# Kernel tuning notes

Measured on AMD Instinct MI355X. Metric: run time of the kernel, lower is better.

## Reference

```python
import jax, jax.numpy as jnp
import numpy as np

TEMPERATURE = 0.07
EPS = 1e-12  # matches torch F.normalize default


def _l2_normalize(x):
    # torch F.normalize: x / max(||x||_2, eps)
    norm = jnp.sqrt(jnp.sum(x * x, axis=-1, keepdims=True))
    return x / jnp.maximum(norm, EPS)


def setup_inputs() -> dict:
    key = jax.random.key(0)
    k1, k2, k3 = jax.random.split(key, 3)
    B, N, D = 4096, 127, 256
    anchor = jax.random.normal(k1, (B, D), dtype=jnp.float32)
    positive = jax.random.normal(k2, (B, D), dtype=jnp.float32)
    negatives = jax.random.normal(k3, (B, N, D), dtype=jnp.float32)
    return {"anchor": anchor, "positive": positive, "negatives": negatives}


def reference(anchor, positive, negatives):
    a = _l2_normalize(anchor)          # [B, D]
    p = _l2_normalize(positive)        # [B, D]
    n = _l2_normalize(negatives)       # [B, N, D]
    pos_scores = jnp.sum(a * p, axis=-1, keepdims=True)   # [B, 1]
    neg_scores = jnp.einsum("bd,bnd->bn", a, n)           # [B, N]
    logits = jnp.concatenate([pos_scores, neg_scores], axis=1) / TEMPERATURE
    # cross-entropy with label 0 for every row
    loss = jnp.mean(jax.nn.logsumexp(logits, axis=-1) - logits[:, 0])
    return loss
```

## Files before the change

kernel.cpp:

```cpp
#include <hip/hip_runtime.h>
#include <math.h>


namespace {
constexpr int B = 4096;
constexpr int N = 127;
constexpr int D = 256;
constexpr float INV_TEMP = 1.0f / 0.07f;
constexpr float EPS = 1e-12f;

__device__ __forceinline__ float wave_reduce_sum(float v) {
    #pragma unroll
    for (int off = 32; off > 0; off >>= 1) v += __shfl_xor(v, off, 64);
    return v;
}

__device__ __forceinline__ float wave_reduce_max(float v) {
    #pragma unroll
    for (int off = 32; off > 0; off >>= 1) v = fmaxf(v, __shfl_xor(v, off, 64));
    return v;
}
}

__global__ __launch_bounds__(256) void infonce_rows(
    const float* __restrict__ anchor,
    const float* __restrict__ positive,
    const float* __restrict__ negatives,
    float* __restrict__ row_loss)
{
    const int b    = blockIdx.x;
    const int tid  = threadIdx.x;
    const int wave = tid >> 6;
    const int lane = tid & 63;

    __shared__ float scores[1 + N];

    const float4 a4 = *reinterpret_cast<const float4*>(
        anchor + (size_t)b * D + lane * 4);
    float asq = a4.x * a4.x + a4.y * a4.y + a4.z * a4.z + a4.w * a4.w;
    asq = wave_reduce_sum(asq);
    const float ainv = 1.0f / fmaxf(sqrtf(asq), EPS);
    const float4 ah = make_float4(a4.x * ainv, a4.y * ainv,
                                  a4.z * ainv, a4.w * ainv);

    if (wave == 0) {
        const float4 p4 = *reinterpret_cast<const float4*>(
            positive + (size_t)b * D + lane * 4);
        float psq  = p4.x * p4.x + p4.y * p4.y + p4.z * p4.z + p4.w * p4.w;
        float pdot = ah.x * p4.x + ah.y * p4.y + ah.z * p4.z + ah.w * p4.w;
        psq  = wave_reduce_sum(psq);
        pdot = wave_reduce_sum(pdot);
        if (lane == 0)
            scores[0] = pdot / fmaxf(sqrtf(psq), EPS);
    }

    const float* nrow_base = negatives + (size_t)b * N * D;
    for (int j = wave; j < N; j += 4) {
        const float4 n4 = *reinterpret_cast<const float4*>(
            nrow_base + (size_t)j * D + lane * 4);
        float nsq  = n4.x * n4.x + n4.y * n4.y + n4.z * n4.z + n4.w * n4.w;
        float ndot = ah.x * n4.x + ah.y * n4.y + ah.z * n4.z + ah.w * n4.w;
        nsq  = wave_reduce_sum(nsq);
        ndot = wave_reduce_sum(ndot);
        if (lane == 0)
            scores[1 + j] = ndot / fmaxf(sqrtf(nsq), EPS);
    }
    __syncthreads();

    if (wave == 0) {
        const float s0 = scores[lane]      * INV_TEMP;
        const float s1 = scores[lane + 64] * INV_TEMP;
        float m = wave_reduce_max(fmaxf(s0, s1));
        float e = expf(s0 - m) + expf(s1 - m);
        e = wave_reduce_sum(e);
        if (lane == 0)
            row_loss[b] = m + logf(e) - scores[0] * INV_TEMP;
    }
}

__global__ __launch_bounds__(256) void reduce_mean(
    const float* __restrict__ row_loss, float* __restrict__ out)
{
    __shared__ float wsum[4];
    const int tid  = threadIdx.x;
    const int wave = tid >> 6;
    const int lane = tid & 63;

    float s = 0.0f;
    for (int i = tid; i < B; i += 256) s += row_loss[i];
    s = wave_reduce_sum(s);
    if (lane == 0) wsum[wave] = s;
    __syncthreads();
    if (tid == 0)
        out[0] = (wsum[0] + wsum[1] + wsum[2] + wsum[3]) * (1.0f / (float)B);
}

extern "C" void kernel_launch(void* const* d_in, const int* in_sizes, int n_in,
                              void* d_out, int out_size, void* d_ws, size_t ws_size,
                              hipStream_t stream) {
    const float* anchor    = (const float*)d_in[0];
    const float* positive  = (const float*)d_in[1];
    const float* negatives = (const float*)d_in[2];
    float* out      = (float*)d_out;
    float* row_loss = (float*)d_ws;

    infonce_rows<<<B, 256, 0, stream>>>(anchor, positive, negatives, row_loss);
    reduce_mean<<<1, 256, 0, stream>>>(row_loss, out);
}
```

Before: 691.2 us.

## Map each vector to a 16-lane group with register prefetch of next vector

Restructures the per-row kernel so each 16-lane group processes a whole 256-float vector with four float4 loads per lane, and double-buffers the next vector's loads in registers while computing the current one. The positive vector is folded into the same loop as slot zero. This raises loads in flight per thread and shortens shuffle reductions, targeting memory latency stalls. It costs more registers per thread.

```diff
diff --git a/kernel.cpp b/kernel.cpp
--- a/kernel.cpp
+++ b/kernel.cpp
@@ -6,15 +6,20 @@
 constexpr int B = 4096;
 constexpr int N = 127;
 constexpr int D = 256;
+constexpr int V = N + 1;
 constexpr float INV_TEMP = 1.0f / 0.07f;
 constexpr float EPS = 1e-12f;
 
+__device__ __forceinline__ float group16_reduce_sum(float v) {
+    #pragma unroll
+    for (int off = 1; off < 16; off <<= 1) v += __shfl_xor(v, off, 64);
+    return v;
+}
 __device__ __forceinline__ float wave_reduce_sum(float v) {
     #pragma unroll
     for (int off = 32; off > 0; off >>= 1) v += __shfl_xor(v, off, 64);
     return v;
 }
-
 __device__ __forceinline__ float wave_reduce_max(float v) {
     #pragma unroll
     for (int off = 32; off > 0; off >>= 1) v = fmaxf(v, __shfl_xor(v, off, 64));
@@ -30,44 +35,67 @@
 {
     const int b    = blockIdx.x;
     const int tid  = threadIdx.x;
-    const int wave = tid >> 6;
     const int lane = tid & 63;
+    const int sub  = lane & 15;
+    const int g    = tid >> 4;
 
-    __shared__ float scores[1 + N];
+    __shared__ float scores[V];
 
-    const float4 a4 = *reinterpret_cast<const float4*>(
-        anchor + (size_t)b * D + lane * 4);
-    float asq = a4.x * a4.x + a4.y * a4.y + a4.z * a4.z + a4.w * a4.w;
-    asq = wave_reduce_sum(asq);
+    const float* arow = anchor + (size_t)b * D;
+    float4 aa[4];
+    #pragma unroll
+    for (int i = 0; i < 4; ++i)
+        aa[i] = *reinterpret_cast<const float4*>(arow + i * 64 + sub * 4);
+    float asq = 0.f;
+    #pragma unroll
+    for (int i = 0; i < 4; ++i)
+        asq += aa[i].x*aa[i].x + aa[i].y*aa[i].y + aa[i].z*aa[i].z + aa[i].w*aa[i].w;
+    asq = group16_reduce_sum(asq);
     const float ainv = 1.0f / fmaxf(sqrtf(asq), EPS);
-    const float4 ah = make_float4(a4.x * ainv, a4.y * ainv,
-                                  a4.z * ainv, a4.w * ainv);
-
-    if (wave == 0) {
-        const float4 p4 = *reinterpret_cast<const float4*>(
-            positive + (size_t)b * D + lane * 4);
-        float psq  = p4.x * p4.x + p4.y * p4.y + p4.z * p4.z + p4.w * p4.w;
-        float pdot = ah.x * p4.x + ah.y * p4.y + ah.z * p4.z + ah.w * p4.w;
-        psq  = wave_reduce_sum(psq);
-        pdot = wave_reduce_sum(pdot);
-        if (lane == 0)
-            scores[0] = pdot / fmaxf(sqrtf(psq), EPS);
+    #pragma unroll
+    for (int i = 0; i < 4; ++i) {
+        aa[i].x *= ainv; aa[i].y *= ainv; aa[i].z *= ainv; aa[i].w *= ainv;
     }
 
-    const float* nrow_base = negatives + (size_t)b * N * D;
-    for (int j = wave; j < N; j += 4) {
-        const float4 n4 = *reinterpret_cast<const float4*>(
-            nrow_base + (size_t)j * D + lane * 4);
-        float nsq  = n4.x * n4.x + n4.y * n4.y + n4.z * n4.z + n4.w * n4.w;
-        float ndot = ah.x * n4.x + ah.y * n4.y + ah.z * n4.z + ah.w * n4.w;
-        nsq  = wave_reduce_sum(nsq);
-        ndot = wave_reduce_sum(ndot);
-        if (lane == 0)
-            scores[1 + j] = ndot / fmaxf(sqrtf(nsq), EPS);
+    auto vec_ptr = [&](int v) -> const float* {
+        return (v == 0) ? (positive + (size_t)b * D)
+                        : (negatives + ((size_t)b * N + (size_t)(v - 1)) * D);
+    };
+
+    float4 cur[4];
+    {
+        const float* p = vec_ptr(g);
+        #pragma unroll
+        for (int i = 0; i < 4; ++i)
+            cur[i] = *reinterpret_cast<const float4*>(p + i * 64 + sub * 4);
+    }
+    #pragma unroll
+    for (int it = 0; it < 8; ++it) {
+        float4 nxt[4];
+        if (it < 7) {
+            const float* p = vec_ptr(g + 16 * (it + 1));
+            #pragma unroll
+            for (int i = 0; i < 4; ++i)
+                nxt[i] = *reinterpret_cast<const float4*>(p + i * 64 + sub * 4);
+        }
+        float ndot = 0.f, nsq = 0.f;
+        #pragma unroll
+        for (int i = 0; i < 4; ++i) {
+            ndot += aa[i].x*cur[i].x + aa[i].y*cur[i].y
+                  + aa[i].z*cur[i].z + aa[i].w*cur[i].w;
+            nsq  += cur[i].x*cur[i].x + cur[i].y*cur[i].y
+                  + cur[i].z*cur[i].z + cur[i].w*cur[i].w;
+        }
+        ndot = group16_reduce_sum(ndot);
+        nsq  = group16_reduce_sum(nsq);
+        if (sub == 0)
+            scores[g + 16 * it] = ndot / fmaxf(sqrtf(nsq), EPS);
+        #pragma unroll
+        for (int i = 0; i < 4; ++i) cur[i] = nxt[i];
     }
     __syncthreads();
 
-    if (wave == 0) {
+    if (tid < 64) {
         const float s0 = scores[lane]      * INV_TEMP;
         const float s1 = scores[lane + 64] * INV_TEMP;
         float m = wave_reduce_max(fmaxf(s0, s1));
```

New measurement: 681.4 us. About the same (-1.4%).
